# Kernel tuning notes

Measured on AMD Instinct MI355X. Metric: run time of the kernel, lower is better.

The kernel has to match this reference:

```python
import jax, jax.numpy as jnp
import numpy as np


def _gcn(x, src, dst, W, b, n):
    # symmetric normalization: deg computed on edges WITH self-loops (weights 1)
    deg = jax.ops.segment_sum(jnp.ones_like(src, dtype=x.dtype), dst, num_segments=n)
    dinv = jnp.where(deg > 0, jax.lax.rsqrt(deg), 0.0)
    norm = dinv[src] * dinv[dst]              # [E+n]
    xw = x @ W                                # [n, out] transform first (cheaper)
    msg = xw[src] * norm[:, None]             # gather + edge scale
    return jax.ops.segment_sum(msg, dst, num_segments=n) + b


def setup_inputs() -> dict:
    key = jax.random.key(0)
    ks = jax.random.split(key, 8)
    N, E = 100_000, 1_280_000
    x = jax.random.normal(ks[0], (N, 18), dtype=jnp.float32)
    edge_index = jax.random.randint(ks[1], (2, E), 0, N, dtype=jnp.int32)
    W1 = jax.random.normal(ks[2], (18, 32), dtype=jnp.float32) * 0.2
    b1 = jnp.zeros((32,), dtype=jnp.float32)
    W2 = jax.random.normal(ks[3], (32, 64), dtype=jnp.float32) * 0.15
    b2 = jnp.zeros((64,), dtype=jnp.float32)
    Wfc = jax.random.normal(ks[4], (64, 2), dtype=jnp.float32) * 0.1
    bfc = jnp.zeros((2,), dtype=jnp.float32)
    return {"x": x, "edge_index": edge_index, "W1": W1, "b1": b1,
            "W2": W2, "b2": b2, "Wfc": Wfc, "bfc": bfc}


def reference(x, edge_index, W1, b1, W2, b2, Wfc, bfc):
    n = x.shape[0]
    loop = jnp.arange(n, dtype=edge_index.dtype)
    src = jnp.concatenate([edge_index[0], loop])   # add self-loops (PyG default)
    dst = jnp.concatenate([edge_index[1], loop])
    h = jax.nn.relu(_gcn(x, src, dst, W1, b1, n))
    h = jax.nn.relu(_gcn(h, src, dst, W2, b2, n))
    logits = h @ Wfc + bfc
    return jax.nn.log_softmax(logits, axis=1)
```

## Files before the change

### kernel.cpp

```cpp
#include <hip/hip_runtime.h>
#include <hip/hip_fp16.h>
#include <math.h>


#define TPB 256
#define BSH 8
#define BNODES 256
#define MAXBUCK 512
#define CH 4096
#define CAPSH 13
#define CAP (1 << CAPSH)

__global__ void k_part(const int* __restrict__ src, const int* __restrict__ dst,
                       int* __restrict__ bcursor, int* __restrict__ eb,
                       __half* __restrict__ u1h, __half* __restrict__ u2h,
                       int E, int n, int nbuck) {
    __shared__ int lh[MAXBUCK];
    __shared__ int lbase[MAXBUCK];
    int t = threadIdx.x;
    if (blockIdx.x == 0 && t < 32) {
        u1h[(size_t)n * 32 + t] = __float2half_rn(0.f);
        u2h[(size_t)n * 32 + t] = __float2half_rn(0.f);
    }
    int chunk0 = blockIdx.x * CH;
    int end = min(chunk0 + CH, E);
    const int4* dst4 = (const int4*)dst;
    const int4* src4 = (const int4*)src;
    for (int i = t; i < nbuck; i += TPB) lh[i] = 0;
    __syncthreads();
    for (int e4 = chunk0 / 4 + t; e4 * 4 < end; e4 += TPB) {
        int base = e4 * 4;
        int4 d = dst4[e4];
        if (base + 0 < end) atomicAdd(&lh[d.x >> BSH], 1);
        if (base + 1 < end) atomicAdd(&lh[d.y >> BSH], 1);
        if (base + 2 < end) atomicAdd(&lh[d.z >> BSH], 1);
        if (base + 3 < end) atomicAdd(&lh[d.w >> BSH], 1);
    }
    __syncthreads();
    for (int i = t; i < nbuck; i += TPB) {
        int c = lh[i];
        lbase[i] = c ? atomicAdd(&bcursor[i], c) : 0;
        lh[i] = 0;
    }
    __syncthreads();
    for (int e4 = chunk0 / 4 + t; e4 * 4 < end; e4 += TPB) {
        int base = e4 * 4;
        int4 d = dst4[e4];
        int4 s = src4[e4];
        #define PUT(c, sv) if (base + c < end) { \
            int b = (d.sv) >> BSH; \
            int r = lbase[b] + atomicAdd(&lh[b], 1); \
            if (r < CAP) \
                eb[((size_t)b << CAPSH) + r] = ((s.sv) << BSH) | ((d.sv) & (BNODES - 1)); }
        PUT(0, x) PUT(1, y) PUT(2, z) PUT(3, w)
        #undef PUT
    }
}

__global__ void k_bucket(const int* __restrict__ eb, const int* __restrict__ bcursor,
                         const float* __restrict__ x, const float* __restrict__ W1,
                         int* __restrict__ csr, int* __restrict__ row_start,
                         int* __restrict__ cnt8, float* __restrict__ dinv,
                         __half* __restrict__ u1h, int n) {
    __shared__ int lcnt[BNODES];
    __shared__ int lscan[BNODES];
    __shared__ float ldinv[BNODES];
    __shared__ float xs[BNODES * 18];
    int b = blockIdx.x;
    int t = threadIdx.x;
    int node0 = b << BSH;
    int beg = b << CAPSH;
    int end = beg + min(bcursor[b], CAP);
    lcnt[t] = 0;
    __syncthreads();
    for (int i = beg + t; i < end; i += TPB)
        atomicAdd(&lcnt[eb[i] & (BNODES - 1)], 1);
    __syncthreads();
    int v = lcnt[t];
    int pad = (v + 7) & ~7;
    lscan[t] = pad;
    __syncthreads();
    for (int off = 1; off < TPB; off <<= 1) {
        int xx = (t >= off) ? lscan[t - off] : 0;
        __syncthreads();
        lscan[t] += xx;
        __syncthreads();
    }
    int pexcl = lscan[t] - pad;
    int node = node0 + t;
    float dv = rsqrtf(1.0f + (float)v);
    ldinv[t] = dv;
    if (node < n) {
        row_start[node] = beg + pexcl;
        cnt8[node] = pad >> 3;
        dinv[node] = dv;
    }
    __syncthreads();
    lcnt[t] = pexcl;
    __syncthreads();
    for (int i = beg + t; i < end; i += TPB) {
        int e = eb[i];
        int p = atomicAdd(&lcnt[e & (BNODES - 1)], 1);
        csr[beg + p] = e >> BSH;
    }
    __syncthreads();
    for (int p = v; p < pad; ++p) csr[beg + pexcl + p] = n;
    int nn = min(BNODES, n - node0);
    const float* xb = x + (size_t)node0 * 18;
    int tot18 = nn * 18;
    for (int i = t; i < tot18; i += TPB) xs[i] = xb[i];
    __syncthreads();
    int f = t & 31, g = t >> 5;
    float w1r[18];
#pragma unroll
    for (int k = 0; k < 18; ++k) w1r[k] = W1[k * 32 + f];
    __half* ub = u1h + (size_t)node0 * 32;
    for (int nl = g; nl < nn; nl += 8) {
        const float* rp = &xs[nl * 18];
        float a = 0.f;
#pragma unroll
        for (int k = 0; k < 18; ++k) a = fmaf(rp[k], w1r[k], a);
        ub[nl * 32 + f] = __float2half_rn(a * ldinv[nl]);
    }
}

#define CVT4(vv, r0, r1, r2, r3) \
    { __half2* _p = (__half2*)&(vv); \
      float2 _fl = __half22float2(_p[0]), _fh = __half22float2(_p[1]); \
      r0 = _fl.x; r1 = _fl.y; r2 = _fh.x; r3 = _fh.y; }

#define GATHER8H(uq, sA, sB, q, a0, a1, a2, a3) \
    { uint2 _v0 = uq[(size_t)(sA).x * 8 + (q)]; \
      uint2 _v1 = uq[(size_t)(sA).y * 8 + (q)]; \
      uint2 _v2 = uq[(size_t)(sA).z * 8 + (q)]; \
      uint2 _v3 = uq[(size_t)(sA).w * 8 + (q)]; \
      uint2 _v4 = uq[(size_t)(sB).x * 8 + (q)]; \
      uint2 _v5 = uq[(size_t)(sB).y * 8 + (q)]; \
      uint2 _v6 = uq[(size_t)(sB).z * 8 + (q)]; \
      uint2 _v7 = uq[(size_t)(sB).w * 8 + (q)]; \
      __half2* _h0 = (__half2*)&_v0; __half2* _h1 = (__half2*)&_v1; \
      __half2* _h2 = (__half2*)&_v2; __half2* _h3 = (__half2*)&_v3; \
      __half2* _h4 = (__half2*)&_v4; __half2* _h5 = (__half2*)&_v5; \
      __half2* _h6 = (__half2*)&_v6; __half2* _h7 = (__half2*)&_v7; \
      __half2 _A01 = __hadd2(_h0[0], _h1[0]), _A23 = __hadd2(_h2[0], _h3[0]); \
      __half2 _A45 = __hadd2(_h4[0], _h5[0]), _A67 = __hadd2(_h6[0], _h7[0]); \
      __half2 _B01 = __hadd2(_h0[1], _h1[1]), _B23 = __hadd2(_h2[1], _h3[1]); \
      __half2 _B45 = __hadd2(_h4[1], _h5[1]), _B67 = __hadd2(_h6[1], _h7[1]); \
      __half2 _A03 = __hadd2(_A01, _A23), _A47 = __hadd2(_A45, _A67); \
      __half2 _B03 = __hadd2(_B01, _B23), _B47 = __hadd2(_B45, _B67); \
      float2 _fa0 = __half22float2(_A03), _fa1 = __half22float2(_A47); \
      float2 _fb0 = __half22float2(_B03), _fb1 = __half22float2(_B47); \
      a0 += _fa0.x + _fa1.x; \
      a1 += _fa0.y + _fa1.y; \
      a2 += _fb0.x + _fb1.x; \
      a3 += _fb0.y + _fb1.y; }

__global__ void k_fused1(const uint2* __restrict__ u1q, const int* __restrict__ row_start,
                         const int* __restrict__ cnt8, const int* __restrict__ csr,
                         const float* __restrict__ dinv,
                         const float* __restrict__ b1, __half* __restrict__ u2h,
                         int n) {
    int t = threadIdx.x;
    int lane = t & 63, wv = t >> 6;
    int q = lane & 7, grp = lane >> 3;
    int node = (blockIdx.x * 4 + wv) * 8 + grp;
    if (node >= n) return;
    float4 bb = ((const float4*)b1)[q];
    uint2 sv = u1q[(size_t)node * 8 + q];
    float a0, a1, a2, a3;
    CVT4(sv, a0, a1, a2, a3)
    int beg = row_start[node];
    int it = cnt8[node];
    const int4* ip = (const int4*)(csr + beg);
    if (it > 0) {
        int4 sA = ip[0], sB = ip[1];
        for (int i = 0; i < it; ++i) {
            int4 nA = ip[2 * i + 2];
            int4 nB = ip[2 * i + 3];
            GATHER8H(u1q, sA, sB, q, a0, a1, a2, a3)
            sA = nA; sB = nB;
        }
    }
    float di = dinv[node];
    float r0 = fmaxf(fmaf(di, a0, bb.x), 0.f) * di;
    float r1 = fmaxf(fmaf(di, a1, bb.y), 0.f) * di;
    float r2 = fmaxf(fmaf(di, a2, bb.z), 0.f) * di;
    float r3 = fmaxf(fmaf(di, a3, bb.w), 0.f) * di;
    uint2 st;
    __half2* sp = (__half2*)&st;
    sp[0].x = __float2half_rn(r0); sp[0].y = __float2half_rn(r1);
    sp[1].x = __float2half_rn(r2); sp[1].y = __float2half_rn(r3);
    ((uint2*)u2h)[(size_t)node * 8 + q] = st;
}

__global__ void k_fused2(const uint2* __restrict__ u2q, const int* __restrict__ row_start,
                         const int* __restrict__ cnt8, const int* __restrict__ csr,
                         const float* __restrict__ dinv,
                         const float* __restrict__ W2,
                         const float* __restrict__ b2, const float* __restrict__ Wfc,
                         const float* __restrict__ bfc, float* __restrict__ out,
                         int n) {
    __shared__ float lagg[4][8][33];
    int t = threadIdx.x;
    int lane = t & 63, wv = t >> 6;
    int q = lane & 7, grp = lane >> 3;
    float w2r[32];
#pragma unroll
    for (int k = 0; k < 32; ++k) w2r[k] = W2[k * 64 + lane];
    float b2v = b2[lane];
    float wf0 = Wfc[lane * 2 + 0], wf1 = Wfc[lane * 2 + 1];
    float bf0 = bfc[0], bf1 = bfc[1];
    int node0 = (blockIdx.x * 4 + wv) * 8;
    int node = node0 + grp;
    float a0 = 0.f, a1 = 0.f, a2 = 0.f, a3 = 0.f;
    if (node < n) {
        uint2 sv = u2q[(size_t)node * 8 + q];
        float s0, s1, s2, s3;
        CVT4(sv, s0, s1, s2, s3)
        a0 = s0; a1 = s1; a2 = s2; a3 = s3;
        int beg = row_start[node];
        int it = cnt8[node];
        const int4* ip = (const int4*)(csr + beg);
        if (it > 0) {
            int4 sA = ip[0], sB = ip[1];
            for (int i = 0; i < it; ++i) {
                int4 nA = ip[2 * i + 2];
                int4 nB = ip[2 * i + 3];
                GATHER8H(u2q, sA, sB, q, a0, a1, a2, a3)
                sA = nA; sB = nB;
            }
        }
    }
    lagg[wv][grp][4 * q + 0] = a0;
    lagg[wv][grp][4 * q + 1] = a1;
    lagg[wv][grp][4 * q + 2] = a2;
    lagg[wv][grp][4 * q + 3] = a3;
#pragma unroll
    for (int r = 0; r < 8; ++r) {
        int nodeT = node0 + r;
        const float* rp = lagg[wv][r];
        float c0 = 0.f, c1 = 0.f, c2 = 0.f, c3 = 0.f;
#pragma unroll
        for (int k = 0; k < 32; k += 4) {
            c0 = fmaf(rp[k],     w2r[k],     c0);
            c1 = fmaf(rp[k + 1], w2r[k + 1], c1);
            c2 = fmaf(rp[k + 2], w2r[k + 2], c2);
            c3 = fmaf(rp[k + 3], w2r[k + 3], c3);
        }
        float a = (c0 + c1) + (c2 + c3);
        float v = (nodeT < n) ? fmaxf(fmaf(dinv[nodeT], a, b2v), 0.f) : 0.f;
        float l0 = v * wf0;
        float l1 = v * wf1;
#pragma unroll
        for (int off = 32; off >= 1; off >>= 1) {
            l0 += __shfl_xor(l0, off, 64);
            l1 += __shfl_xor(l1, off, 64);
        }
        if (lane == 0 && nodeT < n) {
            l0 += bf0;
            l1 += bf1;
            float m2 = fmaxf(l0, l1);
            float lse = m2 + logf(expf(l0 - m2) + expf(l1 - m2));
            out[nodeT * 2 + 0] = l0 - lse;
            out[nodeT * 2 + 1] = l1 - lse;
        }
    }
}

extern "C" void kernel_launch(void* const* d_in, const int* in_sizes, int n_in,
                              void* d_out, int out_size, void* d_ws, size_t ws_size,
                              hipStream_t stream) {
    const float* x   = (const float*)d_in[0];
    const int*   ei  = (const int*)d_in[1];
    const float* W1  = (const float*)d_in[2];
    const float* b1  = (const float*)d_in[3];
    const float* W2  = (const float*)d_in[4];
    const float* b2  = (const float*)d_in[5];
    const float* Wfc = (const float*)d_in[6];
    const float* bfc = (const float*)d_in[7];
    float* out = (float*)d_out;

    const int n = in_sizes[0] / 18;
    const int E = in_sizes[1] / 2;
    const int* src = ei;
    const int* dst = ei + E;
    const int nbuck = (n + BNODES - 1) >> BSH;

    char* w = (char*)d_ws;
    int*    bcursor   = (int*)w;     w += (size_t)nbuck * 4;
    int*    row_start = (int*)w;     w += (size_t)n * 4;
    int*    cnt8      = (int*)w;     w += (size_t)n * 4;
    float*  dinv      = (float*)w;   w += (size_t)n * 4;
    int*    eb        = (int*)w;     w += (size_t)nbuck * CAP * 4;
    int*    csr       = (int*)w;     w += (size_t)nbuck * CAP * 4 + 64;
    w = (char*)(((size_t)w + 63) & ~(size_t)63);
    __half* u1h       = (__half*)w;  w += (size_t)(n + 1) * 32 * 2;
    w = (char*)(((size_t)w + 63) & ~(size_t)63);
    __half* u2h       = (__half*)w;  w += (size_t)(n + 1) * 32 * 2;

    hipMemsetAsync(bcursor, 0, (size_t)nbuck * 4, stream);
    k_part<<<(E + CH - 1) / CH, TPB, 0, stream>>>(src, dst, bcursor, eb, u1h, u2h, E, n, nbuck);
    k_bucket<<<nbuck, TPB, 0, stream>>>(eb, bcursor, x, W1, csr, row_start, cnt8,
                                        dinv, u1h, n);

    const int waves = (n + 7) / 8;
    const int blocksF = (waves + 3) / 4;

    k_fused1<<<blocksF, TPB, 0, stream>>>((const uint2*)u1h, row_start, cnt8, csr,
                                          dinv, b1, u2h, n);
    k_fused2<<<blocksF, TPB, 0, stream>>>((const uint2*)u2h, row_start, cnt8, csr,
                                          dinv, W2, b2, Wfc, bfc, out, n);
}
```

Baseline: 169.3 us.

## Double-buffer neighbor gathers and defer W2 register loads past aggregation

Replaces the one-batch-at-a-time gather loop with a software-pipelined loop. Two register buffers of eight neighbor rows alternate, so the next batch's loads are issued before the current batch is accumulated. This hides gather latency at the cost of more live registers. In the second fused kernel, the W2/Wfc/bias register loads move after aggregation, which lowers register pressure during the gather loop, and a __syncthreads is added. The partition chunk size is also halved to launch more blocks, and the CSR padding grows to cover the deeper index prefetch.

```diff
diff --git a/kernel.cpp b/kernel.cpp
--- a/kernel.cpp
+++ b/kernel.cpp
@@ -7,7 +7,7 @@
 #define BSH 8
 #define BNODES 256
 #define MAXBUCK 512
-#define CH 4096
+#define CH 2048
 #define CAPSH 13
 #define CAP (1 << CAPSH)
 
@@ -124,24 +124,23 @@
     }
 }
 
-#define CVT4(vv, r0, r1, r2, r3) \
-    { __half2* _p = (__half2*)&(vv); \
-      float2 _fl = __half22float2(_p[0]), _fh = __half22float2(_p[1]); \
-      r0 = _fl.x; r1 = _fl.y; r2 = _fh.x; r3 = _fh.y; }
-
-#define GATHER8H(uq, sA, sB, q, a0, a1, a2, a3) \
-    { uint2 _v0 = uq[(size_t)(sA).x * 8 + (q)]; \
-      uint2 _v1 = uq[(size_t)(sA).y * 8 + (q)]; \
-      uint2 _v2 = uq[(size_t)(sA).z * 8 + (q)]; \
-      uint2 _v3 = uq[(size_t)(sA).w * 8 + (q)]; \
-      uint2 _v4 = uq[(size_t)(sB).x * 8 + (q)]; \
-      uint2 _v5 = uq[(size_t)(sB).y * 8 + (q)]; \
-      uint2 _v6 = uq[(size_t)(sB).z * 8 + (q)]; \
-      uint2 _v7 = uq[(size_t)(sB).w * 8 + (q)]; \
-      __half2* _h0 = (__half2*)&_v0; __half2* _h1 = (__half2*)&_v1; \
-      __half2* _h2 = (__half2*)&_v2; __half2* _h3 = (__half2*)&_v3; \
-      __half2* _h4 = (__half2*)&_v4; __half2* _h5 = (__half2*)&_v5; \
-      __half2* _h6 = (__half2*)&_v6; __half2* _h7 = (__half2*)&_v7; \
+#define DECL8(P) uint2 P##0, P##1, P##2, P##3, P##4, P##5, P##6, P##7;
+
+#define LOAD8(P, uq, bA, bB, q) \
+    P##0 = uq[(size_t)(bA).x * 8 + (q)]; \
+    P##1 = uq[(size_t)(bA).y * 8 + (q)]; \
+    P##2 = uq[(size_t)(bA).z * 8 + (q)]; \
+    P##3 = uq[(size_t)(bA).w * 8 + (q)]; \
+    P##4 = uq[(size_t)(bB).x * 8 + (q)]; \
+    P##5 = uq[(size_t)(bB).y * 8 + (q)]; \
+    P##6 = uq[(size_t)(bB).z * 8 + (q)]; \
+    P##7 = uq[(size_t)(bB).w * 8 + (q)];
+
+#define ACC8(P, a0, a1, a2, a3) \
+    { __half2* _h0 = (__half2*)&P##0; __half2* _h1 = (__half2*)&P##1; \
+      __half2* _h2 = (__half2*)&P##2; __half2* _h3 = (__half2*)&P##3; \
+      __half2* _h4 = (__half2*)&P##4; __half2* _h5 = (__half2*)&P##5; \
+      __half2* _h6 = (__half2*)&P##6; __half2* _h7 = (__half2*)&P##7; \
       __half2 _A01 = __hadd2(_h0[0], _h1[0]), _A23 = __hadd2(_h2[0], _h3[0]); \
       __half2 _A45 = __hadd2(_h4[0], _h5[0]), _A67 = __hadd2(_h6[0], _h7[0]); \
       __half2 _B01 = __hadd2(_h0[1], _h1[1]), _B23 = __hadd2(_h2[1], _h3[1]); \
@@ -154,6 +153,30 @@
       a1 += _fa0.y + _fa1.y; \
       a2 += _fb0.x + _fb1.x; \
       a3 += _fb0.y + _fb1.y; }
+
+#define AGG_LOOP(uq, ip, it, q, a0, a1, a2, a3) \
+    { DECL8(va) DECL8(vb) \
+      int4 iA = ip[0], iB = ip[1]; \
+      LOAD8(va, uq, iA, iB, q) \
+      int4 jA = ip[2], jB = ip[3]; \
+      int i = 1; \
+      while (true) { \
+          if (i >= it) { ACC8(va, a0, a1, a2, a3) break; } \
+          LOAD8(vb, uq, jA, jB, q) \
+          iA = ip[2 * i + 2]; iB = ip[2 * i + 3]; \
+          ACC8(va, a0, a1, a2, a3) \
+          ++i; \
+          if (i >= it) { ACC8(vb, a0, a1, a2, a3) break; } \
+          LOAD8(va, uq, iA, iB, q) \
+          jA = ip[2 * i + 2]; jB = ip[2 * i + 3]; \
+          ACC8(vb, a0, a1, a2, a3) \
+          ++i; \
+      } }
+
+#define CVT4(vv, r0, r1, r2, r3) \
+    { __half2* _p = (__half2*)&(vv); \
+      float2 _fl = __half22float2(_p[0]), _fh = __half22float2(_p[1]); \
+      r0 = _fl.x; r1 = _fl.y; r2 = _fh.x; r3 = _fh.y; }
 
 __global__ void k_fused1(const uint2* __restrict__ u1q, const int* __restrict__ row_start,
                          const int* __restrict__ cnt8, const int* __restrict__ csr,
@@ -173,13 +196,7 @@
     int it = cnt8[node];
     const int4* ip = (const int4*)(csr + beg);
     if (it > 0) {
-        int4 sA = ip[0], sB = ip[1];
-        for (int i = 0; i < it; ++i) {
-            int4 nA = ip[2 * i + 2];
-            int4 nB = ip[2 * i + 3];
-            GATHER8H(u1q, sA, sB, q, a0, a1, a2, a3)
-            sA = nA; sB = nB;
-        }
+        AGG_LOOP(u1q, ip, it, q, a0, a1, a2, a3)
     }
     float di = dinv[node];
     float r0 = fmaxf(fmaf(di, a0, bb.x), 0.f) * di;
@@ -204,12 +221,6 @@
     int t = threadIdx.x;
     int lane = t & 63, wv = t >> 6;
     int q = lane & 7, grp = lane >> 3;
-    float w2r[32];
-#pragma unroll
-    for (int k = 0; k < 32; ++k) w2r[k] = W2[k * 64 + lane];
-    float b2v = b2[lane];
-    float wf0 = Wfc[lane * 2 + 0], wf1 = Wfc[lane * 2 + 1];
-    float bf0 = bfc[0], bf1 = bfc[1];
     int node0 = (blockIdx.x * 4 + wv) * 8;
     int node = node0 + grp;
     float a0 = 0.f, a1 = 0.f, a2 = 0.f, a3 = 0.f;
@@ -222,19 +233,20 @@
         int it = cnt8[node];
         const int4* ip = (const int4*)(csr + beg);
         if (it > 0) {
-            int4 sA = ip[0], sB = ip[1];
-            for (int i = 0; i < it; ++i) {
-                int4 nA = ip[2 * i + 2];
-                int4 nB = ip[2 * i + 3];
-                GATHER8H(u2q, sA, sB, q, a0, a1, a2, a3)
-                sA = nA; sB = nB;
-            }
+            AGG_LOOP(u2q, ip, it, q, a0, a1, a2, a3)
         }
     }
     lagg[wv][grp][4 * q + 0] = a0;
     lagg[wv][grp][4 * q + 1] = a1;
     lagg[wv][grp][4 * q + 2] = a2;
     lagg[wv][grp][4 * q + 3] = a3;
+    __syncthreads();
+    float w2r[32];
+#pragma unroll
+    for (int k = 0; k < 32; ++k) w2r[k] = W2[k * 64 + lane];
+    float b2v = b2[lane];
+    float wf0 = Wfc[lane * 2 + 0], wf1 = Wfc[lane * 2 + 1];
+    float bf0 = bfc[0], bf1 = bfc[1];
 #pragma unroll
     for (int r = 0; r < 8; ++r) {
         int nodeT = node0 + r;
@@ -292,7 +304,7 @@
     int*    cnt8      = (int*)w;     w += (size_t)n * 4;
     float*  dinv      = (float*)w;   w += (size_t)n * 4;
     int*    eb        = (int*)w;     w += (size_t)nbuck * CAP * 4;
-    int*    csr       = (int*)w;     w += (size_t)nbuck * CAP * 4 + 64;
+    int*    csr       = (int*)w;     w += (size_t)nbuck * CAP * 4 + 128;
     w = (char*)(((size_t)w + 63) & ~(size_t)63);
     __half* u1h       = (__half*)w;  w += (size_t)(n + 1) * 32 * 2;
     w = (char*)(((size_t)w + 63) & ~(size_t)63);
```

New measurement: 177.3 us. 1.05x slower.

## Split x@W1 out of bucket kernel, use wave-shuffle scan, double partition chunk

Applied to the files above, without the earlier changes.

Moves the first-layer transform (x@W1 scaled by dinv) out of the per-bucket CSR build kernel into a separate k_u1 kernel. That kernel runs one small block per 8 nodes, so the matmul spreads across many more blocks than the roughly 391 bucket blocks. The shared-memory Hillis-Steele scan in k_bucket becomes a wavefront shuffle scan with fewer barriers, and the partition chunk size CH is doubled. The cost is one extra kernel launch and a dinv round trip through global memory.

```diff
diff --git a/kernel.cpp b/kernel.cpp
--- a/kernel.cpp
+++ b/kernel.cpp
@@ -7,7 +7,7 @@
 #define BSH 8
 #define BNODES 256
 #define MAXBUCK 512
-#define CH 4096
+#define CH 8192
 #define CAPSH 13
 #define CAP (1 << CAPSH)
 
@@ -58,14 +58,11 @@
 }
 
 __global__ void k_bucket(const int* __restrict__ eb, const int* __restrict__ bcursor,
-                         const float* __restrict__ x, const float* __restrict__ W1,
                          int* __restrict__ csr, int* __restrict__ row_start,
                          int* __restrict__ cnt8, float* __restrict__ dinv,
-                         __half* __restrict__ u1h, int n) {
+                         int n) {
     __shared__ int lcnt[BNODES];
-    __shared__ int lscan[BNODES];
-    __shared__ float ldinv[BNODES];
-    __shared__ float xs[BNODES * 18];
+    __shared__ int wsum[4];
     int b = blockIdx.x;
     int t = threadIdx.x;
     int node0 = b << BSH;
@@ -78,24 +75,26 @@
     __syncthreads();
     int v = lcnt[t];
     int pad = (v + 7) & ~7;
-    lscan[t] = pad;
-    __syncthreads();
-    for (int off = 1; off < TPB; off <<= 1) {
-        int xx = (t >= off) ? lscan[t - off] : 0;
-        __syncthreads();
-        lscan[t] += xx;
-        __syncthreads();
-    }
-    int pexcl = lscan[t] - pad;
+    int lane = t & 63, wv = t >> 6;
+    int val = pad;
+#pragma unroll
+    for (int off = 1; off < 64; off <<= 1) {
+        int y = __shfl_up(val, off, 64);
+        if (lane >= off) val += y;
+    }
+    if (lane == 63) wsum[wv] = val;
+    __syncthreads();
+    int add = 0;
+#pragma unroll
+    for (int w2 = 0; w2 < 4; ++w2) add += (w2 < wv) ? wsum[w2] : 0;
+    int pexcl = val + add - pad;
     int node = node0 + t;
     float dv = rsqrtf(1.0f + (float)v);
-    ldinv[t] = dv;
     if (node < n) {
         row_start[node] = beg + pexcl;
         cnt8[node] = pad >> 3;
         dinv[node] = dv;
     }
-    __syncthreads();
     lcnt[t] = pexcl;
     __syncthreads();
     for (int i = beg + t; i < end; i += TPB) {
@@ -103,25 +102,30 @@
         int p = atomicAdd(&lcnt[e & (BNODES - 1)], 1);
         csr[beg + p] = e >> BSH;
     }
-    __syncthreads();
     for (int p = v; p < pad; ++p) csr[beg + pexcl + p] = n;
-    int nn = min(BNODES, n - node0);
-    const float* xb = x + (size_t)node0 * 18;
-    int tot18 = nn * 18;
-    for (int i = t; i < tot18; i += TPB) xs[i] = xb[i];
+}
+
+__global__ void k_u1(const float* __restrict__ x, const float* __restrict__ W1,
+                     const float* __restrict__ dinv, __half* __restrict__ u1h,
+                     int n) {
+    __shared__ float xs[8 * 18];
+    __shared__ float w1s[18 * 32];
+    int t = threadIdx.x;
+    int node0 = blockIdx.x * 8;
+    int nn = min(8, n - node0);
+    if (nn <= 0) return;
+    int tot = nn * 18;
+    if (t < tot) xs[t] = x[(size_t)node0 * 18 + t];
+    for (int i = t; i < 18 * 32; i += TPB) w1s[i] = W1[i];
     __syncthreads();
     int f = t & 31, g = t >> 5;
-    float w1r[18];
-#pragma unroll
-    for (int k = 0; k < 18; ++k) w1r[k] = W1[k * 32 + f];
-    __half* ub = u1h + (size_t)node0 * 32;
-    for (int nl = g; nl < nn; nl += 8) {
-        const float* rp = &xs[nl * 18];
-        float a = 0.f;
-#pragma unroll
-        for (int k = 0; k < 18; ++k) a = fmaf(rp[k], w1r[k], a);
-        ub[nl * 32 + f] = __float2half_rn(a * ldinv[nl]);
-    }
+    if (g >= nn) return;
+    float dv = dinv[node0 + g];
+    const float* rp = &xs[g * 18];
+    float a = 0.f;
+#pragma unroll
+    for (int k = 0; k < 18; ++k) a = fmaf(rp[k], w1s[k * 32 + f], a);
+    u1h[(size_t)(node0 + g) * 32 + f] = __float2half_rn(a * dv);
 }
 
 #define CVT4(vv, r0, r1, r2, r3) \
@@ -292,7 +296,7 @@
     int*    cnt8      = (int*)w;     w += (size_t)n * 4;
     float*  dinv      = (float*)w;   w += (size_t)n * 4;
     int*    eb        = (int*)w;     w += (size_t)nbuck * CAP * 4;
-    int*    csr       = (int*)w;     w += (size_t)nbuck * CAP * 4 + 64;
+    int*    csr       = (int*)w;     w += (size_t)nbuck * CAP * 4 + 128;
     w = (char*)(((size_t)w + 63) & ~(size_t)63);
     __half* u1h       = (__half*)w;  w += (size_t)(n + 1) * 32 * 2;
     w = (char*)(((size_t)w + 63) & ~(size_t)63);
@@ -300,8 +304,8 @@
 
     hipMemsetAsync(bcursor, 0, (size_t)nbuck * 4, stream);
     k_part<<<(E + CH - 1) / CH, TPB, 0, stream>>>(src, dst, bcursor, eb, u1h, u2h, E, n, nbuck);
-    k_bucket<<<nbuck, TPB, 0, stream>>>(eb, bcursor, x, W1, csr, row_start, cnt8,
-                                        dinv, u1h, n);
+    k_bucket<<<nbuck, TPB, 0, stream>>>(eb, bcursor, csr, row_start, cnt8, dinv, n);
+    k_u1<<<(n + 7) / 8, TPB, 0, stream>>>(x, W1, dinv, u1h, n);
 
     const int waves = (n + 7) / 8;
     const int blocksF = (waves + 3) / 4;
```

Result: slower. 178.0 us (+5.1%).
